# Kernel optimization log

Hardware: AMD Instinct MI355X
Metric: run time of the kernel (lower is better)

The kernel has to match this reference:

```python
import jax, jax.numpy as jnp
import numpy as np

CLOCK_PERIODS = (1, 2, 4, 8)
HIDDEN = 256
NC = len(CLOCK_PERIODS)
NH = NC * HIDDEN            # 1024: full recurrent state width
EMB = 512
VOCAB = 32000
B, T1 = 16, 257             # x is [B, timesteps]; model consumes T = T1-1 steps


def setup_inputs() -> dict:
    key = jax.random.key(0)
    ks = jax.random.split(key, 8)
    stdv = 1.0 / np.sqrt(HIDDEN)
    Wi = jax.random.uniform(ks[0], (EMB, NH), minval=-stdv, maxval=stdv, dtype=jnp.float32)
    # orthogonal init for Wh (as init.orthogonal_)
    g = jax.random.normal(ks[1], (NH, NH), dtype=jnp.float32)
    q, r = jnp.linalg.qr(g)
    Wh = q * jnp.sign(jnp.diagonal(r))[None, :]
    Wo = jax.random.uniform(ks[2], (NH, VOCAB), minval=-stdv, maxval=stdv, dtype=jnp.float32)
    bi = jnp.zeros((NH,), jnp.float32)
    bh = jnp.zeros((NH,), jnp.float32)
    initial_state = jnp.zeros((NH,), jnp.float32)  # learned param (learn_state=True)
    embedding = jax.random.normal(ks[3], (VOCAB + 1, EMB), dtype=jnp.float32)  # +1 mask token
    x = jax.random.randint(ks[4], (B, T1), 0, VOCAB)
    x_sl = jax.random.randint(ks[5], (B,), 128, T1 + 1)
    return {"x": x, "x_sl": x_sl, "Wi": Wi, "Wh": Wh, "Wo": Wo,
            "bi": bi, "bh": bh, "initial_state": initial_state, "embedding": embedding}


def reference(x, x_sl, Wi, Wh, Wo, bi, bh, initial_state, embedding):
    y = x[:, 1:]                      # targets [B, T]
    xin = x[:, :-1]                   # inputs  [B, T]
    sl = x_sl - 1
    Bsz, T = xin.shape

    # block-upper-triangular recurrent mask: col block >= row block
    block = jnp.arange(NH) // HIDDEN
    utri = (block[None, :] >= block[:, None]).astype(Wh.dtype)
    Whm = Wh * utri

    # per-step active units: clock c active at t iff t % period_c == 0
    periods = jnp.repeat(jnp.asarray(CLOCK_PERIODS), HIDDEN)       # [NH]
    active = (jnp.arange(T)[:, None] % periods[None, :]) == 0      # [T, NH]

    emb = embedding[xin]              # [B, T, E]
    xs = jnp.swapaxes(emb, 0, 1)      # [T, B, E]
    h0 = jnp.broadcast_to(initial_state, (Bsz, NH))

    def step(h_prev, inp):
        xt, a = inp                   # xt [B,E], a [NH] bool
        pre = xt @ Wi + bi + h_prev @ Whm + bh
        # equivalent to the source's variable-width mm on the leading `index` columns
        h_new = jnp.where(a[None, :], jnp.tanh(pre), h_prev)
        return h_new, h_new

    _, hs = jax.lax.scan(step, h0, (xs, active))
    h = jnp.swapaxes(hs, 0, 1)        # [B, T, NH]

    logits = h @ Wo                   # NOTE: source forward never adds bo
    logp = jax.nn.log_softmax(logits, axis=-1)
    ll_tok = jnp.take_along_axis(logp, y[..., None], axis=-1)[..., 0]   # [B, T]
    seq_mask = (jnp.arange(T)[None, :] < sl[:, None]).astype(logits.dtype)
    log_prob = (ll_tok * seq_mask).sum(axis=1)                          # [B]
    loss = -log_prob.sum() / sl.sum()
    return loss, logits
```

## Files before the change

### kernel.cpp

```cpp
#include <hip/hip_runtime.h>

typedef __attribute__((ext_vector_type(8))) short short8;
typedef __attribute__((ext_vector_type(4))) float f32x4;

#define LOG2E 1.4426950408889634f

__device__ __forceinline__ unsigned short f2bf(float f){
  unsigned u = __float_as_uint(f);
  unsigned r = u + 0x7fffu + ((u >> 16) & 1u);
  return (unsigned short)(r >> 16);
}

__device__ __forceinline__ float tanh_fast(float x){
  float ax = fabsf(x);
  float e = __builtin_amdgcn_exp2f(ax * (2.0f * LOG2E));
  float r = 1.0f - 2.0f * __builtin_amdgcn_rcpf(e + 1.0f);
  return copysignf(r, x);
}

__device__ __forceinline__ void gload16(const unsigned short* g, unsigned short* l){
  __builtin_amdgcn_global_load_lds((const __attribute__((address_space(1))) unsigned int*)g,
                                   (__attribute__((address_space(3))) unsigned int*)l,
                                   16, 0, 0);
}


__global__ void k_gather_x(const int* __restrict__ x, const float* __restrict__ emb,
                           unsigned short* __restrict__ X)
{
  int row = blockIdx.x;
  int b = row >> 8, t = row & 255;
  int tok = x[b * 257 + t];
  const float* e = emb + (size_t)tok * 512;
  unsigned short* o = X + (size_t)row * 512;
  for (int i = threadIdx.x; i < 512; i += blockDim.x) o[i] = f2bf(e[i]);
}

__global__ void k_init_h0(const float* __restrict__ init, unsigned short* __restrict__ hbuf){
  int i = blockIdx.x * 256 + threadIdx.x;
  int b = i >> 10, u = i & 1023;
  hbuf[(size_t)(b * 257) * 1024 + u] = f2bf(init[u]);
}

__global__ __launch_bounds__(256) void k_transpose(
    const float* __restrict__ src, unsigned short* __restrict__ dst, int R, int C)
{
  __shared__ float tile[64][65];
  int c0 = blockIdx.x << 6, r0 = blockIdx.y << 6;
  int tid = threadIdx.x;
  for (int i = 0; i < 16; i++){
    int e = (i << 8) + tid; int r = e >> 6, c = e & 63;
    tile[r][c] = src[(size_t)(r0 + r) * C + c0 + c];
  }
  __syncthreads();
  for (int i = 0; i < 16; i++){
    int e = (i << 8) + tid; int rr = e >> 6, cc = e & 63;
    dst[(size_t)(c0 + rr) * R + r0 + cc] = f2bf(tile[cc][rr]);
  }
}

__global__ void k_guard(float* __restrict__ out){ if (threadIdx.x == 0) out[0] = 0.f; }

__global__ __launch_bounds__(256) void k_gemm(
    const unsigned short* __restrict__ A, const unsigned short* __restrict__ B,
    float* __restrict__ C, const float* __restrict__ b0, const float* __restrict__ b1,
    int K, int nTiles, int mode, int J, int ldb)
{
  __shared__ unsigned short aT[128 * 32];
  __shared__ unsigned short bT[128 * 32];
  int bid = blockIdx.x;
  int mt = bid / nTiles, nt = bid % nTiles;
  int m0 = mt << 7, n0 = nt << 7;
  int tid = threadIdx.x;
  int lane = tid & 63, wave = tid >> 6;
  int wm = wave >> 1, wn = wave & 1;
  int wbase = tid & ~63;

  const unsigned short* arow[2];
  int kc[2];
  for (int i = 0; i < 2; i++){
    int e = (i << 8) + tid;
    int r = m0 + (e >> 2);
    kc[i] = (e & 3) << 3;
    const unsigned short* p;
    if (mode == 0)      p = A + (size_t)r * 512;
    else if (mode == 1){ int nA = 256 >> J; int bb = r >> (8 - J); int a = r & (nA - 1);
                         p = A + (size_t)(bb * 257 + (a << J)) * 1024; }
    else               { int bb = r >> 8; int t = r & 255;
                         p = A + (size_t)(bb * 257 + t + 1) * 1024; }
    arow[i] = p;
  }
  const unsigned short* brow[2];
  for (int i = 0; i < 2; i++){
    int e = (i << 8) + tid;
    brow[i] = B + (size_t)(n0 + (e >> 2)) * ldb + ((e & 3) << 3);
  }

  f32x4 acc[4][4] = {};

  int kT = K >> 5;
  for (int kt = 0; kt < kT; kt++){
    int k0 = kt << 5;
    __syncthreads();
    for (int i = 0; i < 2; i++)
      gload16(arow[i] + k0 + kc[i], &aT[((i << 8) + wbase) << 3]);
    for (int i = 0; i < 2; i++)
      gload16(brow[i] + k0, &bT[((i << 8) + wbase) << 3]);
    __syncthreads();
    short8 af[4], bf[4];
#pragma unroll
    for (int i = 0; i < 4; i++)
      af[i] = *(const short8*)&aT[((wm << 6) + (i << 4) + (lane & 15)) * 32 + ((lane >> 4) << 3)];
#pragma unroll
    for (int j = 0; j < 4; j++)
      bf[j] = *(const short8*)&bT[((wn << 6) + (j << 4) + (lane & 15)) * 32 + ((lane >> 4) << 3)];
#pragma unroll
    for (int i = 0; i < 4; i++)
#pragma unroll
      for (int j = 0; j < 4; j++)
        acc[i][j] = __builtin_amdgcn_mfma_f32_16x16x32_bf16(af[i], bf[j], acc[i][j], 0, 0, 0);
  }

#pragma unroll
  for (int i = 0; i < 4; i++)
#pragma unroll
    for (int j = 0; j < 4; j++)
#pragma unroll
      for (int r = 0; r < 4; r++){
        int mg = m0 + (wm << 6) + (i << 4) + ((lane >> 4) << 2) + r;
        int ng = n0 + (wn << 6) + (j << 4) + (lane & 15);
        float v = acc[i][j][r];
        if (mode == 0){
          C[(size_t)mg * 1024 + ng] = v + b0[ng] + b1[ng];
        } else if (mode == 1){
          int nA = 256 >> J; int bb = mg >> (8 - J); int a = mg & (nA - 1);
          C[(size_t)(bb * 256 + (a << J)) * 1024 + (J << 8) + ng] += v;
        } else {
          C[(size_t)mg * 32000 + ng] = v;
        }
      }
}

__global__ __launch_bounds__(512) void k_chain(
    const float* __restrict__ Z, unsigned short* __restrict__ hbuf,
    const unsigned short* __restrict__ Wt, const float* __restrict__ init, int J)
{
  __shared__ unsigned short h[16][264];
  const int p = 1 << J;
  int tid = threadIdx.x, lane = tid & 63, wave = tid >> 6;

  for (int i = tid; i < 4096; i += 512){
    int b = i >> 8, c = i & 255;
    h[b][c] = f2bf(init[(J << 8) + c]);
  }

  short8 wf[2][8];
#pragma unroll
  for (int nt = 0; nt < 2; nt++){
    int ncol = (wave << 5) + (nt << 4) + (lane & 15);
    const unsigned short* wr = Wt + (size_t)((J << 8) + ncol) * 1024 + (J << 8) + ((lane >> 4) << 3);
#pragma unroll
    for (int ks = 0; ks < 8; ks++)
      wf[nt][ks] = *(const short8*)(wr + (ks << 5));
  }
  __syncthreads();

  for (int t = 0; t < 256; t += p){
    short8 af[8];
#pragma unroll
    for (int ks = 0; ks < 8; ks++)
      af[ks] = *(const short8*)&h[lane & 15][(ks << 5) + ((lane >> 4) << 3)];

    float zv[2][4];
#pragma unroll
    for (int nt = 0; nt < 2; nt++)
#pragma unroll
      for (int r = 0; r < 4; r++){
        int b = ((lane >> 4) << 2) + r;
        int c = (wave << 5) + (nt << 4) + (lane & 15);
        zv[nt][r] = Z[(size_t)((b << 8) + t) * 1024 + (J << 8) + c];
      }

    f32x4 acc[2] = {};
#pragma unroll
    for (int nt = 0; nt < 2; nt++)
#pragma unroll
      for (int ks = 0; ks < 8; ks++)
        acc[nt] = __builtin_amdgcn_mfma_f32_16x16x32_bf16(af[ks], wf[nt][ks], acc[nt], 0, 0, 0);

    __syncthreads();
#pragma unroll
    for (int nt = 0; nt < 2; nt++)
#pragma unroll
      for (int r = 0; r < 4; r++){
        int b = ((lane >> 4) << 2) + r;
        int c = (wave << 5) + (nt << 4) + (lane & 15);
        h[b][c] = f2bf(tanh_fast(acc[nt][r] + zv[nt][r]));
      }
    __syncthreads();

    for (int q = 0; q < p; q++){
      int ti = t + q + 1;
#pragma unroll
      for (int i = 0; i < 4; i++){
        int d = tid + (i << 9);
        int b = d >> 7, cp = d & 127;
        *(unsigned int*)(hbuf + (size_t)(b * 257 + ti) * 1024 + (J << 8) + (cp << 1)) =
            *(const unsigned int*)&h[b][cp << 1];
      }
    }
  }
}

__global__ __launch_bounds__(256) void k_loss_rows(
    const float* __restrict__ L, const int* __restrict__ x,
    const int* __restrict__ xsl, float* __restrict__ lacc)
{
  int row = blockIdx.x;
  int b = row >> 8, t = row & 255;
  const float* Lr = L + (size_t)row * 32000;
  int tid = threadIdx.x, lane = tid & 63, wave = tid >> 6;
  float m = -3.0e38f, s = 0.f;
  for (int i = tid; i < 32000; i += 256){
    float v = Lr[i];
    float mn = fmaxf(m, v);
    s = s * __builtin_amdgcn_exp2f((m - mn) * LOG2E) + __builtin_amdgcn_exp2f((v - mn) * LOG2E);
    m = mn;
  }
  __shared__ float smax[4], ssum[4];
  float wm_ = m;
  for (int off = 32; off >= 1; off >>= 1) wm_ = fmaxf(wm_, __shfl_xor(wm_, off));
  if (lane == 0) smax[wave] = wm_;
  __syncthreads();
  float M = fmaxf(fmaxf(smax[0], smax[1]), fmaxf(smax[2], smax[3]));
  float sc = s * __builtin_amdgcn_exp2f((m - M) * LOG2E);
  for (int off = 32; off >= 1; off >>= 1) sc += __shfl_xor(sc, off);
  if (lane == 0) ssum[wave] = sc;
  __syncthreads();
  if (tid == 0){
    float S = ssum[0] + ssum[1] + ssum[2] + ssum[3];
    float lse = M + __builtin_amdgcn_logf(S) * 0.6931471805599453f;
    int y = x[b * 257 + t + 1];
    if (t < xsl[b] - 1) atomicAdd(lacc, Lr[y] - lse);
  }
}

__global__ void k_final(const float* __restrict__ lacc, const int* __restrict__ xsl,
                        float* __restrict__ out){
  if (threadIdx.x == 0){
    int ss = 0;
    for (int b = 0; b < 16; b++) ss += xsl[b] - 1;
    out[0] = -lacc[0] / (float)ss;
  }
}

extern "C" void kernel_launch(void* const* d_in, const int* in_sizes, int n_in,
                              void* d_out, int out_size, void* d_ws, size_t ws_size,
                              hipStream_t stream)
{
  const int*   x   = (const int*)d_in[0];
  const int*   xsl = (const int*)d_in[1];
  const float* Wi  = (const float*)d_in[2];
  const float* Wh  = (const float*)d_in[3];
  const float* Wo  = (const float*)d_in[4];
  const float* bi  = (const float*)d_in[5];
  const float* bh  = (const float*)d_in[6];
  const float* ini = (const float*)d_in[7];
  const float* emb = (const float*)d_in[8];
  float* out = (float*)d_out;

  const size_t WS_NEED = 98074628;
  if (ws_size < WS_NEED){
    k_guard<<<1, 64, 0, stream>>>(out);
    return;
  }

  char* ws = (char*)d_ws;
  float*          Z    = (float*)(ws + 0);
  unsigned short* hbuf = (unsigned short*)(ws + 16777216);
  unsigned short* Wt   = (unsigned short*)(ws + 25198592);
  unsigned short* Wit  = (unsigned short*)(ws + 27295744);
  unsigned short* X    = (unsigned short*)(ws + 28344320);
  unsigned short* Wot  = (unsigned short*)(ws + 32538624);
  float*          lacc = (float*)(ws + 98074624);

  hipMemsetAsync(lacc, 0, 4, stream);

  k_gather_x<<<4096, 128, 0, stream>>>(x, emb, X);
  k_init_h0<<<64, 256, 0, stream>>>(ini, hbuf);
  k_transpose<<<dim3(1024 / 64, 512 / 64), 256, 0, stream>>>(Wi, Wit, 512, 1024);
  k_transpose<<<dim3(1024 / 64, 1024 / 64), 256, 0, stream>>>(Wh, Wt, 1024, 1024);
  k_transpose<<<dim3(32000 / 64, 1024 / 64), 256, 0, stream>>>(Wo, Wot, 1024, 32000);

  k_gemm<<<(4096 / 128) * (1024 / 128), 256, 0, stream>>>(X, Wit, Z, bi, bh, 512, 8, 0, 0, 512);

  k_chain<<<1, 512, 0, stream>>>(Z, hbuf, Wt, ini, 0);
  for (int j = 1; j <= 3; j++){
    int nA = 256 >> j;
    int grid = ((16 * nA) / 128) * 2;
    k_gemm<<<grid, 256, 0, stream>>>(hbuf, Wt + (size_t)(256 * j) * 1024, Z,
                                     nullptr, nullptr, 256 * j, 2, 1, j, 1024);
    k_chain<<<1, 512, 0, stream>>>(Z, hbuf, Wt, ini, j);
  }

  k_gemm<<<(4096 / 128) * (32000 / 128), 256, 0, stream>>>(hbuf, Wot, out + 1,
                                   nullptr, nullptr, 1024, 250, 2, 0, 1024);

  k_loss_rows<<<4096, 256, 0, stream>>>(out + 1, x, xsl, lacc);
  k_final<<<1, 64, 0, stream>>>(lacc, xsl, out);
}
```

Measured before the change: 1.894 ms.

## Prefetch next-step Z in recurrence, vectorize loss row reads, reorder output GEMM tiles

The recurrent kernel now loads the input projection for the next active timestep while the current step's MFMA work runs, taking global-load latency off the serial dependency chain. The loss kernel reads logits as float4 with four independent online-softmax accumulators, handling the unaligned head and tail elements separately. The mode-2 GEMM enumerates tiles M-fastest so that consecutive blocks share the same weight column tile. This adds register pressure, and the alignment special-casing must cover every element exactly once.

```diff
diff --git a/kernel.cpp b/kernel.cpp
--- a/kernel.cpp
+++ b/kernel.cpp
@@ -69,7 +69,9 @@
   __shared__ unsigned short aT[128 * 32];
   __shared__ unsigned short bT[128 * 32];
   int bid = blockIdx.x;
-  int mt = bid / nTiles, nt = bid % nTiles;
+  int mt, nt;
+  if (mode == 2){ mt = bid & 31; nt = bid >> 5; }
+  else          { mt = bid / nTiles; nt = bid % nTiles; }
   int m0 = mt << 7, n0 = nt << 7;
   int tid = threadIdx.x;
   int lane = tid & 63, wave = tid >> 6;
@@ -163,6 +165,16 @@
     for (int ks = 0; ks < 8; ks++)
       wf[nt][ks] = *(const short8*)(wr + (ks << 5));
   }
+
+  float zcur[2][4];
+#pragma unroll
+  for (int nt = 0; nt < 2; nt++)
+#pragma unroll
+    for (int r = 0; r < 4; r++){
+      int b = ((lane >> 4) << 2) + r;
+      int c = (wave << 5) + (nt << 4) + (lane & 15);
+      zcur[nt][r] = Z[(size_t)(b << 8) * 1024 + (J << 8) + c];
+    }
   __syncthreads();
 
   for (int t = 0; t < 256; t += p){
@@ -171,14 +183,15 @@
     for (int ks = 0; ks < 8; ks++)
       af[ks] = *(const short8*)&h[lane & 15][(ks << 5) + ((lane >> 4) << 3)];
 
-    float zv[2][4];
+    float znext[2][4];
+    int tn = (t + p) & 255;
 #pragma unroll
     for (int nt = 0; nt < 2; nt++)
 #pragma unroll
       for (int r = 0; r < 4; r++){
         int b = ((lane >> 4) << 2) + r;
         int c = (wave << 5) + (nt << 4) + (lane & 15);
-        zv[nt][r] = Z[(size_t)((b << 8) + t) * 1024 + (J << 8) + c];
+        znext[nt][r] = Z[(size_t)((b << 8) + tn) * 1024 + (J << 8) + c];
       }
 
     f32x4 acc[2] = {};
@@ -195,7 +208,7 @@
       for (int r = 0; r < 4; r++){
         int b = ((lane >> 4) << 2) + r;
         int c = (wave << 5) + (nt << 4) + (lane & 15);
-        h[b][c] = f2bf(tanh_fast(acc[nt][r] + zv[nt][r]));
+        h[b][c] = f2bf(tanh_fast(acc[nt][r] + zcur[nt][r]));
       }
     __syncthreads();
 
@@ -209,6 +222,12 @@
             *(const unsigned int*)&h[b][cp << 1];
       }
     }
+
+#pragma unroll
+    for (int nt = 0; nt < 2; nt++)
+#pragma unroll
+      for (int r = 0; r < 4; r++)
+        zcur[nt][r] = znext[nt][r];
   }
 }
 
@@ -220,13 +239,44 @@
   int b = row >> 8, t = row & 255;
   const float* Lr = L + (size_t)row * 32000;
   int tid = threadIdx.x, lane = tid & 63, wave = tid >> 6;
-  float m = -3.0e38f, s = 0.f;
-  for (int i = tid; i < 32000; i += 256){
-    float v = Lr[i];
-    float mn = fmaxf(m, v);
-    s = s * __builtin_amdgcn_exp2f((m - mn) * LOG2E) + __builtin_amdgcn_exp2f((v - mn) * LOG2E);
-    m = mn;
-  }
+
+  float m4[4] = {-3.0e38f, -3.0e38f, -3.0e38f, -3.0e38f};
+  float s4[4] = {0.f, 0.f, 0.f, 0.f};
+
+  if (tid < 3){
+    float v = Lr[tid];
+    float mn = fmaxf(m4[0], v);
+    s4[0] = s4[0] * __builtin_amdgcn_exp2f((m4[0] - mn) * LOG2E)
+          + __builtin_amdgcn_exp2f((v - mn) * LOG2E);
+    m4[0] = mn;
+  }
+  if (tid == 3){
+    float v = Lr[31999];
+    float mn = fmaxf(m4[1], v);
+    s4[1] = s4[1] * __builtin_amdgcn_exp2f((m4[1] - mn) * LOG2E)
+          + __builtin_amdgcn_exp2f((v - mn) * LOG2E);
+    m4[1] = mn;
+  }
+
+  const float4* L4 = (const float4*)(Lr + 3);
+  for (int i = tid; i < 7999; i += 256){
+    float4 v = L4[i];
+    float vj[4] = {v.x, v.y, v.z, v.w};
+#pragma unroll
+    for (int j = 0; j < 4; j++){
+      float mn = fmaxf(m4[j], vj[j]);
+      s4[j] = s4[j] * __builtin_amdgcn_exp2f((m4[j] - mn) * LOG2E)
+            + __builtin_amdgcn_exp2f((vj[j] - mn) * LOG2E);
+      m4[j] = mn;
+    }
+  }
+
+  float m = fmaxf(fmaxf(m4[0], m4[1]), fmaxf(m4[2], m4[3]));
+  float s = 0.f;
+#pragma unroll
+  for (int j = 0; j < 4; j++)
+    s += s4[j] * __builtin_amdgcn_exp2f((m4[j] - m) * LOG2E);
+
   __shared__ float smax[4], ssum[4];
   float wm_ = m;
   for (int off = 32; off >= 1; off >>= 1) wm_ = fmaxf(wm_, __shfl_xor(wm_, off));
```

Measured after the change: 1.772 ms. 1.07x faster.
